# Kernel optimization log

Measured on AMD Instinct MI355X. Metric: run time of the kernel, lower is better.

## Reference

```python
import jax, jax.numpy as jnp
import numpy as np

HE = 256  # encoder hidden
HD = 256  # decoder hidden


def _orthogonalize(enc):
    # Faithful to orthogonalize_encoder_inputs_new_new_new:
    # for each timestep i: buffer = x[i] - sum_{j<i} (x[i]*x[j])/(x[i]*x[i]) * x[i]
    # (all ops elementwise). The inner sum over j<i is an exclusive cumsum.
    x = jnp.transpose(enc, (1, 0, 2))                       # [T, B, H]
    s = jnp.cumsum(x, axis=0) - x                           # exclusive cumsum over j<i
    out = x - ((x * s) / (x * x)) * x                       # i=0: s=0 -> out=x
    return jnp.transpose(out, (0, 1, 2)), out               # keep [T,B,H] layout


def setup_inputs() -> dict:
    key = jax.random.key(0)
    k1, k2, k3, k4, k5 = jax.random.split(key, 5)
    B, TE, TD = 16, 128, 128
    # keras 'uniform' initializer = RandomUniform(-0.05, 0.05)
    return {
        "encoder_out_seq": jax.random.normal(k1, (B, TE, HE), dtype=jnp.float32),
        "decoder_out_seq": jax.random.normal(k2, (B, TD, HD), dtype=jnp.float32),
        "W_a": jax.random.uniform(k3, (HE, HE), jnp.float32, -0.05, 0.05),
        "U_a": jax.random.uniform(k4, (HD, HE), jnp.float32, -0.05, 0.05),
        "V_a": jax.random.uniform(k5, (HE, 1), jnp.float32, -0.05, 0.05),
    }


def reference(encoder_out_seq, decoder_out_seq, W_a, U_a, V_a):
    # Gram-Schmidt-style pass (math as in source; exactly vectorizable)
    x = jnp.transpose(encoder_out_seq, (1, 0, 2))           # [TE, B, H]
    s = jnp.cumsum(x, axis=0) - x                           # sum_{j<i} x[j]
    ortho = x - ((x * s) / (x * x)) * x                     # [TE, B, H]
    enc = jnp.transpose(ortho, (1, 0, 2))                   # [B, TE, H]

    # Bahdanau attention: the K.rnn steps carry no real state, so vectorize
    # over decoder time.
    was = jnp.einsum('beh,hk->bek', enc, W_a)               # [B, TE, H]
    uah = jnp.einsum('bdh,hk->bdk', decoder_out_seq, U_a)   # [B, TD, H]
    # tanh(S.Wa + h.Ua) . Va  -> energies [B, TD, TE]
    energy = jnp.einsum('bdeh,ho->bde',
                        jnp.tanh(was[:, None, :, :] + uah[:, :, None, :]),
                        V_a)
    e_outputs = jax.nn.softmax(energy, axis=-1)             # [B, TD, TE]
    c_outputs = jnp.einsum('bde,beh->bdh', e_outputs, enc)  # [B, TD, H]
    return c_outputs, e_outputs
```

## Files before the change

### kernel.cpp

```cpp
#include <hip/hip_runtime.h>
#include <cstddef>

#define Bq 16
#define TEq 128
#define TDq 128
#define Hq 256

#define kC2  2.8853900817779268f
#define kL2E 1.4426950408889634f

static __device__ __forceinline__ float fast_rcp(float x) {
#if __has_builtin(__builtin_amdgcn_rcpf)
    return __builtin_amdgcn_rcpf(x);
#else
    return 1.0f / x;
#endif
}

static __device__ __forceinline__ float fast_exp2(float x) {
#if __has_builtin(__builtin_amdgcn_exp2f)
    return __builtin_amdgcn_exp2f(x);
#else
    return exp2f(x);
#endif
}

__global__ __launch_bounds__(64) void k_ortho(const float* __restrict__ enc,
                                              float* __restrict__ out) {
    const int idx = blockIdx.x * 64 + threadIdx.x;
    const int b = idx >> 8;
    const int h = idx & 255;
    const float* p = enc + (size_t)b * TEq * Hq + h;
    float* q = out + (size_t)b * TEq * Hq + h;
    float s = 0.0f;
#pragma unroll 8
    for (int t = 0; t < TEq; ++t) {
        const float x = p[(size_t)t * Hq];
        const float r = (x * s) / (x * x);
        q[(size_t)t * Hq] = x - r * x;
        s += x;
    }
}

__global__ __launch_bounds__(256) void k_gemm2(const float* __restrict__ A0,
                                               const float* __restrict__ A1,
                                               const float* __restrict__ W0,
                                               const float* __restrict__ W1,
                                               float* __restrict__ Cw,
                                               float* __restrict__ Cu) {
    const int z = blockIdx.z;
    const float* __restrict__ A = z ? A1 : A0;
    const float* __restrict__ W = z ? W1 : W0;
    float* __restrict__ C = z ? Cu : Cw;
    const float scale = z ? 1.0f : kC2;

    const int bm = blockIdx.y * 64;
    const int bn = blockIdx.x * 64;

    __shared__ float sA[16][68];
    __shared__ float sB[16][64];

    const int tid = threadIdx.x;
    const int tx = tid & 15;
    const int ty = tid >> 4;
    const int arow = tid >> 2;
    const int akcol = (tid & 3) << 2;
    const int brow = tid >> 4;
    const int bcol = (tid & 15) << 2;

    float acc[4][4] = {};

    for (int k0 = 0; k0 < Hq; k0 += 16) {
        const float4 av = *(const float4*)(A + (size_t)(bm + arow) * Hq + k0 + akcol);
        const float4 bv = *(const float4*)(W + (size_t)(k0 + brow) * Hq + bn + bcol);
        __syncthreads();
        sA[akcol + 0][arow] = av.x;
        sA[akcol + 1][arow] = av.y;
        sA[akcol + 2][arow] = av.z;
        sA[akcol + 3][arow] = av.w;
        *(float4*)&sB[brow][bcol] = bv;
        __syncthreads();
#pragma unroll
        for (int k = 0; k < 16; ++k) {
            const float4 a4 = *(const float4*)&sA[k][ty << 2];
            const float4 b4 = *(const float4*)&sB[k][tx << 2];
            const float aarr[4] = {a4.x, a4.y, a4.z, a4.w};
            const float barr[4] = {b4.x, b4.y, b4.z, b4.w};
#pragma unroll
            for (int i = 0; i < 4; ++i)
#pragma unroll
                for (int j = 0; j < 4; ++j)
                    acc[i][j] = fmaf(aarr[i], barr[j], acc[i][j]);
        }
    }
#pragma unroll
    for (int i = 0; i < 4; ++i) {
        float4 o;
        o.x = acc[i][0] * scale;
        o.y = acc[i][1] * scale;
        o.z = acc[i][2] * scale;
        o.w = acc[i][3] * scale;
        *(float4*)(C + (size_t)(bm + (ty << 2) + i) * Hq + bn + (tx << 2)) = o;
    }
}

__global__ __launch_bounds__(256) void k_attn(const float* __restrict__ was,
                                              const float* __restrict__ uah,
                                              const float* __restrict__ enc_o,
                                              const float* __restrict__ Va,
                                              float* __restrict__ c_out,
                                              float* __restrict__ e_out) {
    const int b = blockIdx.y;
    const int d0 = blockIdx.x << 2;

    __shared__ float uahs[4][Hq];
    __shared__ float Vs[Hq];
    __shared__ float wts[4][TEq];

    const int tid = threadIdx.x;
    const int w = tid >> 6;
    const int lane = tid & 63;

    Vs[tid] = Va[tid];
#pragma unroll
    for (int j = 0; j < 4; ++j)
        uahs[j][tid] = uah[((size_t)b * TDq + d0 + j) * Hq + tid] * kC2;
    __syncthreads();

    const int g = lane >> 4;
    const int ll = lane & 15;

    float vs = Vs[lane] + Vs[lane + 64] + Vs[lane + 128] + Vs[lane + 192];
#pragma unroll
    for (int m = 1; m <= 32; m <<= 1) vs += __shfl_xor(vs, m);

    float4 ur[4], vr[4];
#pragma unroll
    for (int c = 0; c < 4; ++c) {
        ur[c] = *(const float4*)&uahs[w][c * 64 + (ll << 2)];
        vr[c] = *(const float4*)&Vs[c * 64 + (ll << 2)];
    }

    const float* wasb = was + (size_t)b * TEq * Hq;

    for (int ei = 0; ei < 32; ++ei) {
        const int e = (g << 5) + ei;
        const float* wp = wasb + (size_t)e * Hq + (ll << 2);
        float acc = 0.0f;
#pragma unroll
        for (int c = 0; c < 4; ++c) {
            const float4 wv = *(const float4*)(wp + c * 64);
            const float wf[4] = {wv.x, wv.y, wv.z, wv.w};
            const float uf[4] = {ur[c].x, ur[c].y, ur[c].z, ur[c].w};
            const float vf[4] = {vr[c].x, vr[c].y, vr[c].z, vr[c].w};
#pragma unroll
            for (int i = 0; i < 4; ++i) {
                const float s = wf[i] + uf[i];
                const float t = fast_exp2(s);
                const float r = fast_rcp(t + 1.0f);
                acc = fmaf(vf[i], r, acc);
            }
        }
        acc += __shfl_xor(acc, 1);
        acc += __shfl_xor(acc, 2);
        acc += __shfl_xor(acc, 4);
        acc += __shfl_xor(acc, 8);
        if (ll == 0) wts[w][e] = vs - 2.0f * acc;
    }

    float v0 = wts[w][lane];
    float v1 = wts[w][lane + 64];
    float mx = fmaxf(v0, v1);
#pragma unroll
    for (int m = 1; m <= 32; m <<= 1) mx = fmaxf(mx, __shfl_xor(mx, m));
    const float e0 = fast_exp2((v0 - mx) * kL2E);
    const float e1 = fast_exp2((v1 - mx) * kL2E);
    float sm = e0 + e1;
#pragma unroll
    for (int m = 1; m <= 32; m <<= 1) sm += __shfl_xor(sm, m);
    const float inv = fast_rcp(sm);
    const float w0 = e0 * inv;
    const float w1 = e1 * inv;
    wts[w][lane] = w0;
    wts[w][lane + 64] = w1;
    {
        const size_t eb = ((size_t)b * TDq + d0 + w) * TEq;
        e_out[eb + lane] = w0;
        e_out[eb + lane + 64] = w1;
    }
    __syncthreads();

    float a0 = 0.0f, a1 = 0.0f, a2 = 0.0f, a3 = 0.0f;
    const float* ep = enc_o + (size_t)b * TEq * Hq + tid;
#pragma unroll 8
    for (int e = 0; e < TEq; ++e) {
        const float evv = ep[(size_t)e * Hq];
        a0 = fmaf(wts[0][e], evv, a0);
        a1 = fmaf(wts[1][e], evv, a1);
        a2 = fmaf(wts[2][e], evv, a2);
        a3 = fmaf(wts[3][e], evv, a3);
    }
    const size_t cb = ((size_t)b * TDq + d0) * Hq + tid;
    c_out[cb] = a0;
    c_out[cb + Hq] = a1;
    c_out[cb + 2 * Hq] = a2;
    c_out[cb + 3 * Hq] = a3;
}

extern "C" void kernel_launch(void* const* d_in, const int* in_sizes, int n_in,
                              void* d_out, int out_size, void* d_ws, size_t ws_size,
                              hipStream_t stream) {
    const float* enc = (const float*)d_in[0];
    const float* dec = (const float*)d_in[1];
    const float* Wa  = (const float*)d_in[2];
    const float* Ua  = (const float*)d_in[3];
    const float* Va  = (const float*)d_in[4];

    float* c_out = (float*)d_out;
    float* e_out = c_out + (size_t)Bq * TDq * Hq;

    float* enc_o = (float*)d_ws;
    float* wasb  = enc_o + (size_t)Bq * TEq * Hq;
    float* uahb  = wasb + (size_t)Bq * TEq * Hq;

    k_ortho<<<dim3((Bq * Hq) / 64), dim3(64), 0, stream>>>(enc, enc_o);
    k_gemm2<<<dim3(Hq / 64, (Bq * TEq) / 64, 2), dim3(256), 0, stream>>>(
        enc_o, dec, Wa, Ua, wasb, uahb);
    k_attn<<<dim3(TDq / 4, Bq), dim3(256), 0, stream>>>(
        wasb, uahb, enc_o, Va, c_out, e_out);
}
```

Before: 116.4 us.

## Raise parallelism in ortho scan, GEMM tiles, and attention blocks

The orthogonalization pass becomes a two-level chunked scan: each block covers 32 hidden columns, and 8 chunks of 16 timesteps compute partial sums in shared memory. This replaces the fully serial 128-step loop run by only 64 blocks. The GEMM tile shrinks from 64x64 to 32x64, doubling the block count, and the attention kernel handles 2 decoder rows per block instead of 4, with two waves splitting the encoder range per row. The aim is to fill more of the GPU's compute units at the cost of less register reuse per thread and extra barriers.

```diff
diff --git a/kernel.cpp b/kernel.cpp
--- a/kernel.cpp
+++ b/kernel.cpp
@@ -25,19 +25,36 @@
 #endif
 }
 
-__global__ __launch_bounds__(64) void k_ortho(const float* __restrict__ enc,
-                                              float* __restrict__ out) {
-    const int idx = blockIdx.x * 64 + threadIdx.x;
-    const int b = idx >> 8;
-    const int h = idx & 255;
-    const float* p = enc + (size_t)b * TEq * Hq + h;
-    float* q = out + (size_t)b * TEq * Hq + h;
+__global__ __launch_bounds__(256) void k_ortho(const float* __restrict__ enc,
+                                               float* __restrict__ out) {
+    const int b = blockIdx.y;
+    const int hg = blockIdx.x;
+    const int tid = threadIdx.x;
+    const int hl = tid & 31;
+    const int ck = tid >> 5;
+    const int h = (hg << 5) + hl;
+
+    __shared__ float sums[8][33];
+
+    const float* p = enc + ((size_t)b * TEq + ck * 16) * Hq + h;
+    float xs[16];
+#pragma unroll
+    for (int i = 0; i < 16; ++i) xs[i] = p[(size_t)i * Hq];
+    float tot = 0.0f;
+#pragma unroll
+    for (int i = 0; i < 16; ++i) tot += xs[i];
+    sums[ck][hl] = tot;
+    __syncthreads();
+
     float s = 0.0f;
-#pragma unroll 8
-    for (int t = 0; t < TEq; ++t) {
-        const float x = p[(size_t)t * Hq];
+    for (int c = 0; c < ck; ++c) s += sums[c][hl];
+
+    float* q = out + ((size_t)b * TEq + ck * 16) * Hq + h;
+#pragma unroll
+    for (int i = 0; i < 16; ++i) {
+        const float x = xs[i];
         const float r = (x * s) / (x * x);
-        q[(size_t)t * Hq] = x - r * x;
+        q[(size_t)i * Hq] = x - r * x;
         s += x;
     }
 }
@@ -54,53 +71,53 @@
     float* __restrict__ C = z ? Cu : Cw;
     const float scale = z ? 1.0f : kC2;
 
-    const int bm = blockIdx.y * 64;
+    const int bm = blockIdx.y * 32;
     const int bn = blockIdx.x * 64;
 
-    __shared__ float sA[16][68];
+    __shared__ float sA[16][33];
     __shared__ float sB[16][64];
 
     const int tid = threadIdx.x;
     const int tx = tid & 15;
     const int ty = tid >> 4;
-    const int arow = tid >> 2;
-    const int akcol = (tid & 3) << 2;
+    const int arow = tid >> 3;
+    const int akcol = (tid & 7) << 1;
     const int brow = tid >> 4;
     const int bcol = (tid & 15) << 2;
 
-    float acc[4][4] = {};
+    float acc[2][4] = {};
 
     for (int k0 = 0; k0 < Hq; k0 += 16) {
-        const float4 av = *(const float4*)(A + (size_t)(bm + arow) * Hq + k0 + akcol);
+        const float2 av = *(const float2*)(A + (size_t)(bm + arow) * Hq + k0 + akcol);
         const float4 bv = *(const float4*)(W + (size_t)(k0 + brow) * Hq + bn + bcol);
         __syncthreads();
         sA[akcol + 0][arow] = av.x;
         sA[akcol + 1][arow] = av.y;
-        sA[akcol + 2][arow] = av.z;
-        sA[akcol + 3][arow] = av.w;
         *(float4*)&sB[brow][bcol] = bv;
         __syncthreads();
 #pragma unroll
         for (int k = 0; k < 16; ++k) {
-            const float4 a4 = *(const float4*)&sA[k][ty << 2];
+            const float a0 = sA[k][ty << 1];
+            const float a1 = sA[k][(ty << 1) + 1];
             const float4 b4 = *(const float4*)&sB[k][tx << 2];
-            const float aarr[4] = {a4.x, a4.y, a4.z, a4.w};
-            const float barr[4] = {b4.x, b4.y, b4.z, b4.w};
-#pragma unroll
-            for (int i = 0; i < 4; ++i)
-#pragma unroll
-                for (int j = 0; j < 4; ++j)
-                    acc[i][j] = fmaf(aarr[i], barr[j], acc[i][j]);
+            acc[0][0] = fmaf(a0, b4.x, acc[0][0]);
+            acc[0][1] = fmaf(a0, b4.y, acc[0][1]);
+            acc[0][2] = fmaf(a0, b4.z, acc[0][2]);
+            acc[0][3] = fmaf(a0, b4.w, acc[0][3]);
+            acc[1][0] = fmaf(a1, b4.x, acc[1][0]);
+            acc[1][1] = fmaf(a1, b4.y, acc[1][1]);
+            acc[1][2] = fmaf(a1, b4.z, acc[1][2]);
+            acc[1][3] = fmaf(a1, b4.w, acc[1][3]);
         }
     }
 #pragma unroll
-    for (int i = 0; i < 4; ++i) {
+    for (int i = 0; i < 2; ++i) {
         float4 o;
         o.x = acc[i][0] * scale;
         o.y = acc[i][1] * scale;
         o.z = acc[i][2] * scale;
         o.w = acc[i][3] * scale;
-        *(float4*)(C + (size_t)(bm + (ty << 2) + i) * Hq + bn + (tx << 2)) = o;
+        *(float4*)(C + (size_t)(bm + (ty << 1) + i) * Hq + bn + (tx << 2)) = o;
     }
 }
 
@@ -111,19 +128,21 @@
                                               float* __restrict__ c_out,
                                               float* __restrict__ e_out) {
     const int b = blockIdx.y;
-    const int d0 = blockIdx.x << 2;
-
-    __shared__ float uahs[4][Hq];
+    const int d0 = blockIdx.x << 1;
+
+    __shared__ float uahs[2][Hq];
     __shared__ float Vs[Hq];
-    __shared__ float wts[4][TEq];
+    __shared__ float wts[2][TEq];
 
     const int tid = threadIdx.x;
     const int w = tid >> 6;
     const int lane = tid & 63;
+    const int dl = w >> 1;
+    const int half = w & 1;
 
     Vs[tid] = Va[tid];
 #pragma unroll
-    for (int j = 0; j < 4; ++j)
+    for (int j = 0; j < 2; ++j)
         uahs[j][tid] = uah[((size_t)b * TDq + d0 + j) * Hq + tid] * kC2;
     __syncthreads();
 
@@ -137,14 +156,14 @@
     float4 ur[4], vr[4];
 #pragma unroll
     for (int c = 0; c < 4; ++c) {
-        ur[c] = *(const float4*)&uahs[w][c * 64 + (ll << 2)];
+        ur[c] = *(const float4*)&uahs[dl][c * 64 + (ll << 2)];
         vr[c] = *(const float4*)&Vs[c * 64 + (ll << 2)];
     }
 
     const float* wasb = was + (size_t)b * TEq * Hq;
 
-    for (int ei = 0; ei < 32; ++ei) {
-        const int e = (g << 5) + ei;
+    for (int ei = 0; ei < 16; ++ei) {
+        const int e = (half << 6) + (g << 4) + ei;
         const float* wp = wasb + (size_t)e * Hq + (ll << 2);
         float acc = 0.0f;
 #pragma unroll
@@ -165,46 +184,43 @@
         acc += __shfl_xor(acc, 2);
         acc += __shfl_xor(acc, 4);
         acc += __shfl_xor(acc, 8);
-        if (ll == 0) wts[w][e] = vs - 2.0f * acc;
-    }
-
-    float v0 = wts[w][lane];
-    float v1 = wts[w][lane + 64];
-    float mx = fmaxf(v0, v1);
-#pragma unroll
-    for (int m = 1; m <= 32; m <<= 1) mx = fmaxf(mx, __shfl_xor(mx, m));
-    const float e0 = fast_exp2((v0 - mx) * kL2E);
-    const float e1 = fast_exp2((v1 - mx) * kL2E);
-    float sm = e0 + e1;
-#pragma unroll
-    for (int m = 1; m <= 32; m <<= 1) sm += __shfl_xor(sm, m);
-    const float inv = fast_rcp(sm);
-    const float w0 = e0 * inv;
-    const float w1 = e1 * inv;
-    wts[w][lane] = w0;
-    wts[w][lane + 64] = w1;
-    {
+        if (ll == 0) wts[dl][e] = vs - 2.0f * acc;
+    }
+    __syncthreads();
+
+    if (w < 2) {
+        const float v0 = wts[w][lane];
+        const float v1 = wts[w][lane + 64];
+        float mx = fmaxf(v0, v1);
+#pragma unroll
+        for (int m = 1; m <= 32; m <<= 1) mx = fmaxf(mx, __shfl_xor(mx, m));
+        const float e0 = fast_exp2((v0 - mx) * kL2E);
+        const float e1 = fast_exp2((v1 - mx) * kL2E);
+        float sm = e0 + e1;
+#pragma unroll
+        for (int m = 1; m <= 32; m <<= 1) sm += __shfl_xor(sm, m);
+        const float inv = fast_rcp(sm);
+        const float w0 = e0 * inv;
+        const float w1 = e1 * inv;
+        wts[w][lane] = w0;
+        wts[w][lane + 64] = w1;
         const size_t eb = ((size_t)b * TDq + d0 + w) * TEq;
         e_out[eb + lane] = w0;
         e_out[eb + lane + 64] = w1;
     }
     __syncthreads();
 
-    float a0 = 0.0f, a1 = 0.0f, a2 = 0.0f, a3 = 0.0f;
+    float a0 = 0.0f, a1 = 0.0f;
     const float* ep = enc_o + (size_t)b * TEq * Hq + tid;
 #pragma unroll 8
     for (int e = 0; e < TEq; ++e) {
         const float evv = ep[(size_t)e * Hq];
         a0 = fmaf(wts[0][e], evv, a0);
         a1 = fmaf(wts[1][e], evv, a1);
-        a2 = fmaf(wts[2][e], evv, a2);
-        a3 = fmaf(wts[3][e], evv, a3);
     }
     const size_t cb = ((size_t)b * TDq + d0) * Hq + tid;
     c_out[cb] = a0;
     c_out[cb + Hq] = a1;
-    c_out[cb + 2 * Hq] = a2;
-    c_out[cb + 3 * Hq] = a3;
 }
 
 extern "C" void kernel_launch(void* const* d_in, const int* in_sizes, int n_in,
@@ -223,9 +239,9 @@
     float* wasb  = enc_o + (size_t)Bq * TEq * Hq;
     float* uahb  = wasb + (size_t)Bq * TEq * Hq;
 
-    k_ortho<<<dim3((Bq * Hq) / 64), dim3(64), 0, stream>>>(enc, enc_o);
-    k_gemm2<<<dim3(Hq / 64, (Bq * TEq) / 64, 2), dim3(256), 0, stream>>>(
+    k_ortho<<<dim3(Hq / 32, Bq), dim3(256), 0, stream>>>(enc, enc_o);
+    k_gemm2<<<dim3(Hq / 64, (Bq * TEq) / 32, 2), dim3(256), 0, stream>>>(
         enc_o, dec, Wa, Ua, wasb, uahb);
-    k_attn<<<dim3(TDq / 4, Bq), dim3(256), 0, stream>>>(
+    k_attn<<<dim3(TDq / 2, Bq), dim3(256), 0, stream>>>(
         wasb, uahb, enc_o, Va, c_out, e_out);
 }
```

Result: faster. 106.2 us (-8.7%).
